# Optimization experiments

Measured on AMD Instinct MI355X. Metric: run time of the kernel, lower is better.

Reference implementation:

```python
import jax, jax.numpy as jnp
import numpy as np

N_LAGS = 64
UNBIASED = False


def setup_inputs() -> dict:
    key = jax.random.key(0)
    X = jax.random.normal(key, (4096, 8192), dtype=jnp.float32)
    return {"X": X}


def reference(X) -> jnp.ndarray:
    # X: [B, T]
    B, T = X.shape
    Xc = X - jnp.mean(X, axis=1, keepdims=True)  # center per sequence
    acs = []
    for k in range(N_LAGS + 1):  # small fixed loop over lags
        denom = (T - k) if UNBIASED else T
        # sum_{t} Xc[b, t] * Xc[b, t+k]
        ac_k = jnp.einsum('bt,bt->b', Xc[:, : T - k], Xc[:, k:]) / denom
        acs.append(ac_k)
    Xautocorr = jnp.stack(acs, axis=1)  # [B, n_lags+1]
    # normalize lags 1..n_lags by lag-0 variance
    return Xautocorr[:, 1:] / Xautocorr[:, :1]
```

## Files before the change

### kernel.cpp

```cpp
#include <hip/hip_runtime.h>


typedef __bf16 bf16x8 __attribute__((ext_vector_type(8)));
typedef float f32x16 __attribute__((ext_vector_type(16)));
typedef unsigned int uint32;

#define T_LEN 8192
#define WPB 4
#define GB_STRIDE 34
#define GB_SHORTS (96 * GB_STRIDE)

__device__ __forceinline__ uint32 pack2bf(float a, float b) {
  uint32 ua = __builtin_bit_cast(uint32, a);
  uint32 ub = __builtin_bit_cast(uint32, b);
  ua += 0x7fffu + ((ua >> 16) & 1u);
  ub += 0x7fffu + ((ub >> 16) & 1u);
  return (ua >> 16) | (ub & 0xffff0000u);
}
__device__ __forceinline__ short f2bf(float f) {
  uint32 u = __builtin_bit_cast(uint32, f);
  return (short)((u + 0x7fffu + ((u >> 16) & 1u)) >> 16);
}
__device__ __forceinline__ float bf2f(short h) {
  uint32 u = ((uint32)(unsigned short)h) << 16;
  return __builtin_bit_cast(float, u);
}

__global__ __launch_bounds__(WPB * 64, 4)
void autocorr_kernel(const float* __restrict__ X, float* __restrict__ out, int nrows) {
  __shared__ short gb_all[WPB * GB_SHORTS];
  const int wave = threadIdx.x >> 6;
  const int lane = threadIdx.x & 63;
  const int row = blockIdx.x * WPB + wave;
  if (row >= nrows) return;
  short* gb = gb_all + wave * GB_SHORTS;

  const int m = lane & 31;
  const int sh = lane >> 5;
  const float* __restrict__ base = X + (size_t)row * T_LEN + (sh << 8) + m;

  f32x16 g0 = {}, g1 = {}, g2 = {};
  float ssum = 0.f;

#define CHUNK_BODY(PP, E8, E9)                                                  \
  {                                                                             \
    float e0 = (PP)[0],   e1 = (PP)[32],  e2 = (PP)[64],  e3 = (PP)[96];        \
    float e4 = (PP)[128], e5 = (PP)[160], e6 = (PP)[192], e7 = (PP)[224];       \
    float e8 = (E8), e9 = (E9);                                                 \
    ssum += ((e0 + e1) + (e2 + e3)) + ((e4 + e5) + (e6 + e7));                  \
    uint32 u0 = pack2bf(e0, e1), u1 = pack2bf(e2, e3), u2 = pack2bf(e4, e5);    \
    uint32 u3 = pack2bf(e6, e7), u4 = pack2bf(e8, e9);                          \
    int4 a4 = make_int4((int)u0, (int)u1, (int)u2, (int)u3);                    \
    int4 b1;                                                                    \
    b1.x = (int)((u0 >> 16) | (u1 << 16));                                      \
    b1.y = (int)((u1 >> 16) | (u2 << 16));                                      \
    b1.z = (int)((u2 >> 16) | (u3 << 16));                                      \
    b1.w = (int)((u3 >> 16) | (u4 << 16));                                      \
    int4 b2 = make_int4((int)u1, (int)u2, (int)u3, (int)u4);                    \
    bf16x8 fa = __builtin_bit_cast(bf16x8, a4);                                 \
    bf16x8 f1 = __builtin_bit_cast(bf16x8, b1);                                 \
    bf16x8 f2 = __builtin_bit_cast(bf16x8, b2);                                 \
    g0 = __builtin_amdgcn_mfma_f32_32x32x16_bf16(fa, fa, g0, 0, 0, 0);          \
    g1 = __builtin_amdgcn_mfma_f32_32x32x16_bf16(fa, f1, g1, 0, 0, 0);          \
    g2 = __builtin_amdgcn_mfma_f32_32x32x16_bf16(fa, f2, g2, 0, 0, 0);          \
  }

#pragma unroll 3
  for (int c = 0; c < 15; ++c) {
    const float* p = base + (c << 9);
    CHUNK_BODY(p, p[256], p[288])
  }
  {
    const float* p = base + (15 << 9);
    float e8s = 0.f, e9s = 0.f;
    if (!sh) { e8s = p[256]; e9s = p[288]; }
    CHUNK_BODY(p, e8s, e9s)
  }
#undef CHUNK_BODY

  for (int d = 32; d > 0; d >>= 1) ssum += __shfl_xor(ssum, d, 64);

#pragma unroll
  for (int v = 0; v < 16; ++v) {
    int rm = (v & 3) + (sh << 2) + ((v >> 2) << 3);
    gb[(rm)      * GB_STRIDE + m] = f2bf(g0[v]);
    gb[(32 + rm) * GB_STRIDE + m] = f2bf(g1[v]);
    gb[(64 + rm) * GB_STRIDE + m] = f2bf(g2[v]);
  }

  int k = lane + 1;
  int s2 = k & 31, q = k >> 5;
  float ck = 0.f;
#pragma unroll 4
  for (int mm = 0; mm < 32; ++mm) {
    int ms = mm + s2;
    int dd = q + (ms >> 5);
    ck += bf2f(gb[(dd * 32 + mm) * GB_STRIDE + (ms & 31)]);
  }
  float c0 = 0.f;
#pragma unroll 4
  for (int mm = 0; mm < 32; ++mm) c0 += bf2f(gb[mm * GB_STRIDE + mm]);

  float P = X[(size_t)row * T_LEN + lane];
  float Q = X[(size_t)row * T_LEN + (T_LEN - 1 - lane)];
  for (int d = 1; d < 64; d <<= 1) {
    float tp = __shfl_up(P, (unsigned)d, 64);
    float tq = __shfl_up(Q, (unsigned)d, 64);
    if (lane >= d) { P += tp; Q += tq; }
  }
  float mu = ssum * (1.0f / (float)T_LEN);
  float Ck = ck - mu * (2.f * ssum - P - Q) + (float)(T_LEN - k) * mu * mu;
  float C0 = c0 - mu * 2.f * ssum + (float)T_LEN * mu * mu;
  out[(size_t)row * 64 + lane] = Ck / C0;
}

extern "C" void kernel_launch(void* const* d_in, const int* in_sizes, int n_in,
                              void* d_out, int out_size, void* d_ws, size_t ws_size,
                              hipStream_t stream) {
  const float* X = (const float*)d_in[0];
  float* out = (float*)d_out;
  int nrows = in_sizes[0] / T_LEN;
  dim3 grid((nrows + WPB - 1) / WPB);
  autocorr_kernel<<<grid, dim3(WPB * 64), 0, stream>>>(X, out, nrows);
}
```

Before: 188.7 us.

## Replace halo loads with cross-lane shuffle, hardware bf16 pack, and register prefetch

Each lane used to reload the two halo elements (p[256], p[288]) from global memory. These are now obtained by packing the next chunk's first pair and exchanging it with the other half-wave through a shuffle, which removes the redundant loads. The manual round-to-nearest bf16 packing is replaced with the v_cvt_pk_bf16_f32 instruction. The loop is software-pipelined so the next chunk's loads are issued before the current chunk's MFMAs. In exchange, each iteration adds a cross-lane shuffle and holds more live registers, which could lower occupancy.

After: 189.3 us. No clear change (+0.3%).

```diff
diff --git a/kernel.cpp b/kernel.cpp
--- a/kernel.cpp
+++ b/kernel.cpp
@@ -10,12 +10,10 @@
 #define GB_STRIDE 34
 #define GB_SHORTS (96 * GB_STRIDE)
 
-__device__ __forceinline__ uint32 pack2bf(float a, float b) {
-  uint32 ua = __builtin_bit_cast(uint32, a);
-  uint32 ub = __builtin_bit_cast(uint32, b);
-  ua += 0x7fffu + ((ua >> 16) & 1u);
-  ub += 0x7fffu + ((ub >> 16) & 1u);
-  return (ua >> 16) | (ub & 0xffff0000u);
+__device__ __forceinline__ uint32 cvtpk(float lo, float hi) {
+  uint32 r;
+  asm("v_cvt_pk_bf16_f32 %0, %1, %2" : "=v"(r) : "v"(lo), "v"(hi));
+  return r;
 }
 __device__ __forceinline__ short f2bf(float f) {
   uint32 u = __builtin_bit_cast(uint32, f);
@@ -42,41 +40,42 @@
   f32x16 g0 = {}, g1 = {}, g2 = {};
   float ssum = 0.f;
 
-#define CHUNK_BODY(PP, E8, E9)                                                  \
-  {                                                                             \
-    float e0 = (PP)[0],   e1 = (PP)[32],  e2 = (PP)[64],  e3 = (PP)[96];        \
-    float e4 = (PP)[128], e5 = (PP)[160], e6 = (PP)[192], e7 = (PP)[224];       \
-    float e8 = (E8), e9 = (E9);                                                 \
-    ssum += ((e0 + e1) + (e2 + e3)) + ((e4 + e5) + (e6 + e7));                  \
-    uint32 u0 = pack2bf(e0, e1), u1 = pack2bf(e2, e3), u2 = pack2bf(e4, e5);    \
-    uint32 u3 = pack2bf(e6, e7), u4 = pack2bf(e8, e9);                          \
-    int4 a4 = make_int4((int)u0, (int)u1, (int)u2, (int)u3);                    \
-    int4 b1;                                                                    \
-    b1.x = (int)((u0 >> 16) | (u1 << 16));                                      \
-    b1.y = (int)((u1 >> 16) | (u2 << 16));                                      \
-    b1.z = (int)((u2 >> 16) | (u3 << 16));                                      \
-    b1.w = (int)((u3 >> 16) | (u4 << 16));                                      \
-    int4 b2 = make_int4((int)u1, (int)u2, (int)u3, (int)u4);                    \
-    bf16x8 fa = __builtin_bit_cast(bf16x8, a4);                                 \
-    bf16x8 f1 = __builtin_bit_cast(bf16x8, b1);                                 \
-    bf16x8 f2 = __builtin_bit_cast(bf16x8, b2);                                 \
-    g0 = __builtin_amdgcn_mfma_f32_32x32x16_bf16(fa, fa, g0, 0, 0, 0);          \
-    g1 = __builtin_amdgcn_mfma_f32_32x32x16_bf16(fa, f1, g1, 0, 0, 0);          \
-    g2 = __builtin_amdgcn_mfma_f32_32x32x16_bf16(fa, f2, g2, 0, 0, 0);          \
+  float e0 = base[0],   e1 = base[32],  e2 = base[64],  e3 = base[96];
+  float e4 = base[128], e5 = base[160], e6 = base[192], e7 = base[224];
+  uint32 u0 = cvtpk(e0, e1);
+
+#pragma unroll 4
+  for (int c = 0; c < 16; ++c) {
+    float n0 = 0.f, n1 = 0.f, n2 = 0.f, n3 = 0.f;
+    float n4 = 0.f, n5 = 0.f, n6 = 0.f, n7 = 0.f;
+    if (c < 15) {
+      const float* pn = base + ((c + 1) << 9);
+      n0 = pn[0];   n1 = pn[32];  n2 = pn[64];  n3 = pn[96];
+      n4 = pn[128]; n5 = pn[160]; n6 = pn[192]; n7 = pn[224];
+    }
+
+    ssum += ((e0 + e1) + (e2 + e3)) + ((e4 + e5) + (e6 + e7));
+    uint32 u1 = cvtpk(e2, e3), u2 = cvtpk(e4, e5), u3 = cvtpk(e6, e7);
+    uint32 u0n = cvtpk(n0, n1);
+    uint32 u4 = (uint32)__shfl_xor((int)(sh ? u0 : u0n), 32, 64);
+
+    int4 a4 = make_int4((int)u0, (int)u1, (int)u2, (int)u3);
+    int4 b1;
+    b1.x = (int)((u0 >> 16) | (u1 << 16));
+    b1.y = (int)((u1 >> 16) | (u2 << 16));
+    b1.z = (int)((u2 >> 16) | (u3 << 16));
+    b1.w = (int)((u3 >> 16) | (u4 << 16));
+    int4 b2 = make_int4((int)u1, (int)u2, (int)u3, (int)u4);
+    bf16x8 fa = __builtin_bit_cast(bf16x8, a4);
+    bf16x8 f1 = __builtin_bit_cast(bf16x8, b1);
+    bf16x8 f2 = __builtin_bit_cast(bf16x8, b2);
+    g0 = __builtin_amdgcn_mfma_f32_32x32x16_bf16(fa, fa, g0, 0, 0, 0);
+    g1 = __builtin_amdgcn_mfma_f32_32x32x16_bf16(fa, f1, g1, 0, 0, 0);
+    g2 = __builtin_amdgcn_mfma_f32_32x32x16_bf16(fa, f2, g2, 0, 0, 0);
+
+    e0 = n0; e1 = n1; e2 = n2; e3 = n3; e4 = n4; e5 = n5; e6 = n6; e7 = n7;
+    u0 = u0n;
   }
-
-#pragma unroll 3
-  for (int c = 0; c < 15; ++c) {
-    const float* p = base + (c << 9);
-    CHUNK_BODY(p, p[256], p[288])
-  }
-  {
-    const float* p = base + (15 << 9);
-    float e8s = 0.f, e9s = 0.f;
-    if (!sh) { e8s = p[256]; e9s = p[288]; }
-    CHUNK_BODY(p, e8s, e9s)
-  }
-#undef CHUNK_BODY
 
   for (int d = 32; d > 0; d >>= 1) ssum += __shfl_xor(ssum, d, 64);
 
```

## Software-pipeline row loads two chunks ahead and use hardware bf16 pack conversion

Applied to the files above, without the earlier changes.

The main loop is fully unrolled with a rotating register buffer, so loads for chunk c+2 are issued while chunk c is converted and fed to the MFMAs. This hides global memory latency inside each wave. It also swaps the manual round-to-nearest bf16 packing for the v_cvt_pk_bf16_f32 instruction, which cuts the VALU work per element. The cost is higher register pressure from 20 extra live floats, which could hurt occupancy under the launch bound of 4.

Measured after the change: 213.3 us. 1.13x slower.

```diff
diff --git a/kernel.cpp b/kernel.cpp
--- a/kernel.cpp
+++ b/kernel.cpp
@@ -10,12 +10,10 @@
 #define GB_STRIDE 34
 #define GB_SHORTS (96 * GB_STRIDE)
 
-__device__ __forceinline__ uint32 pack2bf(float a, float b) {
-  uint32 ua = __builtin_bit_cast(uint32, a);
-  uint32 ub = __builtin_bit_cast(uint32, b);
-  ua += 0x7fffu + ((ua >> 16) & 1u);
-  ub += 0x7fffu + ((ub >> 16) & 1u);
-  return (ua >> 16) | (ub & 0xffff0000u);
+__device__ __forceinline__ uint32 cvtpk(float lo, float hi) {
+  uint32 r;
+  asm("v_cvt_pk_bf16_f32 %0, %1, %2" : "=v"(r) : "v"(lo), "v"(hi));
+  return r;
 }
 __device__ __forceinline__ short f2bf(float f) {
   uint32 u = __builtin_bit_cast(uint32, f);
@@ -25,6 +23,44 @@
   uint32 u = ((uint32)(unsigned short)h) << 16;
   return __builtin_bit_cast(float, u);
 }
+
+#define DECL10(V) float V##0, V##1, V##2, V##3, V##4, V##5, V##6, V##7, V##8, V##9;
+
+#define LOAD10(V, c) {                                                          \
+    const float* p = base + ((c) << 9);                                         \
+    V##0 = p[0];   V##1 = p[32];  V##2 = p[64];  V##3 = p[96];                  \
+    V##4 = p[128]; V##5 = p[160]; V##6 = p[192]; V##7 = p[224];                 \
+    V##8 = p[256]; V##9 = p[288]; }
+
+#define LOAD10_LAST(V) {                                                        \
+    const float* p = base + (15 << 9);                                          \
+    V##0 = p[0];   V##1 = p[32];  V##2 = p[64];  V##3 = p[96];                  \
+    V##4 = p[128]; V##5 = p[160]; V##6 = p[192]; V##7 = p[224];                 \
+    V##8 = 0.f; V##9 = 0.f;                                                     \
+    if (!sh) { V##8 = p[256]; V##9 = p[288]; } }
+
+#define COMPUTE10(V) {                                                          \
+    ssum += ((V##0 + V##1) + (V##2 + V##3)) + ((V##4 + V##5) + (V##6 + V##7));  \
+    uint32 u0 = cvtpk(V##0, V##1), u1 = cvtpk(V##2, V##3);                      \
+    uint32 u2 = cvtpk(V##4, V##5), u3 = cvtpk(V##6, V##7);                      \
+    uint32 u4 = cvtpk(V##8, V##9);                                              \
+    int4 a4 = make_int4((int)u0, (int)u1, (int)u2, (int)u3);                    \
+    int4 b1;                                                                    \
+    b1.x = (int)((u0 >> 16) | (u1 << 16));                                      \
+    b1.y = (int)((u1 >> 16) | (u2 << 16));                                      \
+    b1.z = (int)((u2 >> 16) | (u3 << 16));                                      \
+    b1.w = (int)((u3 >> 16) | (u4 << 16));                                      \
+    int4 b2 = make_int4((int)u1, (int)u2, (int)u3, (int)u4);                    \
+    bf16x8 fa = __builtin_bit_cast(bf16x8, a4);                                 \
+    bf16x8 f1 = __builtin_bit_cast(bf16x8, b1);                                 \
+    bf16x8 f2 = __builtin_bit_cast(bf16x8, b2);                                 \
+    g0 = __builtin_amdgcn_mfma_f32_32x32x16_bf16(fa, fa, g0, 0, 0, 0);          \
+    g1 = __builtin_amdgcn_mfma_f32_32x32x16_bf16(fa, f1, g1, 0, 0, 0);          \
+    g2 = __builtin_amdgcn_mfma_f32_32x32x16_bf16(fa, f2, g2, 0, 0, 0); }
+
+#define ROT10(D, S) { D##0 = S##0; D##1 = S##1; D##2 = S##2; D##3 = S##3;       \
+                      D##4 = S##4; D##5 = S##5; D##6 = S##6; D##7 = S##7;       \
+                      D##8 = S##8; D##9 = S##9; }
 
 __global__ __launch_bounds__(WPB * 64, 4)
 void autocorr_kernel(const float* __restrict__ X, float* __restrict__ out, int nrows) {
@@ -42,41 +78,20 @@
   f32x16 g0 = {}, g1 = {}, g2 = {};
   float ssum = 0.f;
 
-#define CHUNK_BODY(PP, E8, E9)                                                  \
-  {                                                                             \
-    float e0 = (PP)[0],   e1 = (PP)[32],  e2 = (PP)[64],  e3 = (PP)[96];        \
-    float e4 = (PP)[128], e5 = (PP)[160], e6 = (PP)[192], e7 = (PP)[224];       \
-    float e8 = (E8), e9 = (E9);                                                 \
-    ssum += ((e0 + e1) + (e2 + e3)) + ((e4 + e5) + (e6 + e7));                  \
-    uint32 u0 = pack2bf(e0, e1), u1 = pack2bf(e2, e3), u2 = pack2bf(e4, e5);    \
-    uint32 u3 = pack2bf(e6, e7), u4 = pack2bf(e8, e9);                          \
-    int4 a4 = make_int4((int)u0, (int)u1, (int)u2, (int)u3);                    \
-    int4 b1;                                                                    \
-    b1.x = (int)((u0 >> 16) | (u1 << 16));                                      \
-    b1.y = (int)((u1 >> 16) | (u2 << 16));                                      \
-    b1.z = (int)((u2 >> 16) | (u3 << 16));                                      \
-    b1.w = (int)((u3 >> 16) | (u4 << 16));                                      \
-    int4 b2 = make_int4((int)u1, (int)u2, (int)u3, (int)u4);                    \
-    bf16x8 fa = __builtin_bit_cast(bf16x8, a4);                                 \
-    bf16x8 f1 = __builtin_bit_cast(bf16x8, b1);                                 \
-    bf16x8 f2 = __builtin_bit_cast(bf16x8, b2);                                 \
-    g0 = __builtin_amdgcn_mfma_f32_32x32x16_bf16(fa, fa, g0, 0, 0, 0);          \
-    g1 = __builtin_amdgcn_mfma_f32_32x32x16_bf16(fa, f1, g1, 0, 0, 0);          \
-    g2 = __builtin_amdgcn_mfma_f32_32x32x16_bf16(fa, f2, g2, 0, 0, 0);          \
+  DECL10(A) DECL10(B)
+  LOAD10(A, 0)
+  LOAD10(B, 1)
+
+#pragma unroll
+  for (int c = 0; c < 16; ++c) {
+    DECL10(N)
+    N0 = N1 = N2 = N3 = N4 = N5 = N6 = N7 = N8 = N9 = 0.f;
+    if (c + 2 < 15)       LOAD10(N, c + 2)
+    else if (c + 2 == 15) LOAD10_LAST(N)
+    COMPUTE10(A)
+    ROT10(A, B)
+    ROT10(B, N)
   }
-
-#pragma unroll 3
-  for (int c = 0; c < 15; ++c) {
-    const float* p = base + (c << 9);
-    CHUNK_BODY(p, p[256], p[288])
-  }
-  {
-    const float* p = base + (15 << 9);
-    float e8s = 0.f, e9s = 0.f;
-    if (!sh) { e8s = p[256]; e9s = p[288]; }
-    CHUNK_BODY(p, e8s, e9s)
-  }
-#undef CHUNK_BODY
 
   for (int d = 32; d > 0; d >>= 1) ssum += __shfl_xor(ssum, d, 64);
 
```
